# Optimization experiments

Hardware: AMD Instinct MI355X
Metric: run time of the kernel (lower is better)

## Reference

```python
import jax, jax.numpy as jnp
from jax import lax
import numpy as np

EPS_COS = 1e-8   # cosine-similarity eps (matches F.cosine_similarity default scale)
EPS_IN = 1e-5    # InstanceNorm2d default eps
NEG = -1e9


def _conv3(x, w, b):
    # x: [B,C,H,W], w: [O,I,3,3]
    y = lax.conv_general_dilated(x, w, (1, 1), 'SAME',
                                 dimension_numbers=('NCHW', 'OIHW', 'NCHW'))
    return y + b[None, :, None, None]


def _inorm(x):
    m = jnp.mean(x, axis=(2, 3), keepdims=True)
    v = jnp.var(x, axis=(2, 3), keepdims=True)
    return (x - m) * lax.rsqrt(v + EPS_IN)


def _shift(former, latter, mask):
    # former/latter: [B,C,H,W]; mask: [H,W] int (1 = hole).
    # For every masked pixel, find the most cosine-similar UNMASKED pixel in the
    # latter (known-region encoder) features and copy the former feature from it.
    B, C, H, W = former.shape
    L = H * W
    lat = lax.stop_gradient(latter).reshape(B, C, L)           # attention is non-differentiable
    latn = lat / (jnp.linalg.norm(lat, axis=1, keepdims=True) + EPS_COS)
    sim = jnp.einsum('bcm,bcn->bmn', latn, latn)               # [B,L,L] query m -> key n
    mflat = mask.reshape(L) > 0
    sim = jnp.where(mflat[None, None, :], NEG, sim)            # keys must be unmasked
    idx = jnp.argmax(sim, axis=-1)                             # [B,L]
    fflat = former.reshape(B, C, L)
    gathered = jnp.take_along_axis(fflat, jnp.broadcast_to(idx[:, None, :], (B, C, L)), axis=2)
    shift = jnp.where(mflat[None, None, :], gathered, 0.0)     # zeros outside the hole
    return shift.reshape(B, C, H, W)


def setup_inputs() -> dict:
    key = jax.random.key(0)
    ks = jax.random.split(key, 6)
    B, C, H, W = 8, 256, 64, 64
    inp = jax.random.normal(ks[0], (B, 2 * C, H, W), dtype=jnp.float32)
    mask = jax.random.randint(ks[1], (H, W), 0, 2, dtype=jnp.int32)
    s1 = 1.0 / float(np.sqrt(2 * C * 9))
    s2 = 1.0 / float(np.sqrt(C * 9))
    W1 = jax.random.uniform(ks[2], (C, 2 * C, 3, 3), jnp.float32, -s1, s1)
    b1 = jax.random.uniform(ks[3], (C,), jnp.float32, -s1, s1)
    W2 = jax.random.uniform(ks[4], (C, C, 3, 3), jnp.float32, -s2, s2)
    b2 = jax.random.uniform(ks[5], (C,), jnp.float32, -s2, s2)
    return {"input": inp, "mask": mask, "W1": W1, "b1": b1, "W2": W2, "b2": b2}


def reference(input, mask, W1, b1, W2, b2):
    C = input.shape[1] // 2
    F_c = input[:, :C]          # former (decoder) features
    F_s = input[:, C:]          # latter (encoder) features
    F_shift = _shift(F_c, F_s, mask)
    F_fuse = F_c * F_shift
    F_com = jnp.concatenate([F_c, F_fuse], axis=1)             # [B,2C,H,W]
    h = jax.nn.relu(_inorm(_conv3(F_com, W1, b1)))
    res = _inorm(_conv3(h, W2, b2))
    return jnp.concatenate([F_c + res, F_s], axis=1)
```

## Files before the change

### kernel.cpp

```cpp
#include <hip/hip_runtime.h>
#include <hip/hip_bf16.h>
#include <math.h>

#define L 4096
#define C 256
#define B 8

typedef __attribute__((ext_vector_type(8))) short bf16x8;
typedef __attribute__((ext_vector_type(8))) ushort u16x8;
typedef __attribute__((ext_vector_type(4))) float f32x4;

__device__ inline ushort f2bu(float f) { __hip_bfloat16 h = __float2bfloat16(f); return *(ushort*)&h; }
__device__ inline float bu2f(ushort u) { __hip_bfloat16 h; *(ushort*)&h = u; return __bfloat162float(h); }

#define SWZ(c) ((((c) >> 1) & 3) << 4)

__global__ __launch_bounds__(256) void compact_mask(
    const int* __restrict__ mask, int* __restrict__ counts,
    int* __restrict__ maskedOrig, int* __restrict__ unmaskOrig,
    int* __restrict__ posOf)
{
    __shared__ int smM[256], smU[256];
    int t = threadIdx.x;
    int flags[16];
    int cm = 0, cu = 0;
    for (int k = 0; k < 16; ++k) {
        int l = t * 16 + k;
        int f = mask[l] > 0;
        flags[k] = f;
        cm += f; cu += !f;
    }
    smM[t] = cm; smU[t] = cu;
    __syncthreads();
    for (int off = 1; off < 256; off <<= 1) {
        int vM = 0, vU = 0;
        if (t >= off) { vM = smM[t - off]; vU = smU[t - off]; }
        __syncthreads();
        smM[t] += vM; smU[t] += vU;
        __syncthreads();
    }
    if (t == 255) { counts[0] = smM[255]; counts[1] = smU[255]; }
    int pm = smM[t] - cm, pu = smU[t] - cu;
    for (int k = 0; k < 16; ++k) {
        int l = t * 16 + k;
        if (flags[k]) { maskedOrig[pm] = l; posOf[l] = pm; pm++; }
        else          { unmaskOrig[pu] = l; posOf[l] = pu; pu++; }
    }
}

__global__ __launch_bounds__(256) void norm_transpose(
    const float* __restrict__ input, const int* __restrict__ mask,
    const int* __restrict__ counts, const int* __restrict__ posOf,
    ushort* __restrict__ fsnh, ushort* __restrict__ fsnl)
{
    int bx = blockIdx.x;
    int b = bx >> 7;
    int l0 = (bx & 127) * 32;
    __shared__ float tile[256 * 33];
    __shared__ float part[8 * 33];
    __shared__ float denom[32];
    __shared__ int   rowdst[32];
    int t = threadIdx.x;
    int lsub = t & 31, cg = t >> 5;
    for (int cc = 0; cc < 256; cc += 8) {
        int c = cc + cg;
        tile[c * 33 + lsub] = input[((size_t)(b * 512 + 256 + c)) * L + l0 + lsub];
    }
    __syncthreads();
    float s = 0.f;
    for (int c = cg; c < 256; c += 8) { float v = tile[c * 33 + lsub]; s = fmaf(v, v, s); }
    part[cg * 33 + lsub] = s;
    __syncthreads();
    if (t < 32) {
        float s2 = 0.f;
        for (int g = 0; g < 8; ++g) s2 += part[g * 33 + t];
        denom[t] = sqrtf(s2) + 1e-8f;
        int l = l0 + t;
        int Nm = counts[0];
        rowdst[t] = (mask[l] > 0) ? posOf[l] : (Nm + posOf[l]);
    }
    __syncthreads();
    for (int ls = 0; ls < 32; ++ls) {
        int r = rowdst[ls];
        float d = denom[ls];
        float val = tile[t * 33 + ls] / d;
        ushort h = f2bu(val);
        float hf = bu2f(h);
        ushort lo = f2bu(val - hf);
        size_t o = ((size_t)b * L + r) * C + t;
        fsnh[o] = h;
        fsnl[o] = lo;
    }
}

__global__ __launch_bounds__(256, 2) void sim_argmax_v6(
    const ushort* __restrict__ hi, const ushort* __restrict__ lo,
    const int* __restrict__ counts,
    float* __restrict__ pval, int* __restrict__ pidx)
{
    __shared__ ushort ldsB[2 * 64 * 256];
    const int Nm = counts[0], Nu = counts[1];
    const int b = blockIdx.z;
    const int m0 = blockIdx.y * 64;
    const int half = blockIdx.x;
    const int t = threadIdx.x;
    const int w = t >> 6, l = t & 63;
    const int lm = l & 15, lk = l >> 4;
    const int key = lm << 4;

    const int nct = (Nu + 63) >> 6;
    const int hs = (nct + 1) >> 1;
    const int cA = half * hs, cB = half ? nct : hs;

    float bestv[4]; int bestn[4];
#pragma unroll
    for (int r = 0; r < 4; ++r) { bestv[r] = -3e38f; bestn[r] = 0; }

    if (m0 < Nm && cA < cB) {
        const char* bytesH = (const char*)hi;
        const char* bytesL = (const char*)lo;
        const size_t bL = (size_t)b * L;
        char* ldsc = (char*)ldsB;

#define STAGE(cc) do { \
    size_t gb = (bL + (size_t)Nm + (size_t)(cc) * 64) * 512; \
    _Pragma("unroll") \
    for (int i = 0; i < 8; ++i) { \
        int j = w * 8 + i; \
        int x = j * 1024 + l * 16; \
        int sx = x ^ (((x >> 9) & 15) << 4); \
        __builtin_amdgcn_global_load_lds((const __attribute__((address_space(1))) unsigned*)(bytesH + gb + sx), \
            (__attribute__((address_space(3))) unsigned*)(ldsc + j * 1024), 16, 0, 0); \
        __builtin_amdgcn_global_load_lds((const __attribute__((address_space(1))) unsigned*)(bytesL + gb + sx), \
            (__attribute__((address_space(3))) unsigned*)(ldsc + 32768 + j * 1024), 16, 0, 0); \
    } \
} while (0)

        STAGE(cA);

        const int rA = m0 + w * 16 + lm;
        bf16x8 ah[8], al[8];
        {
            const ushort* aH = hi + (bL + rA) * C + lk * 8;
            const ushort* aL = lo + (bL + rA) * C + lk * 8;
#pragma unroll
            for (int ks = 0; ks < 8; ++ks) {
                ah[ks] = *(const bf16x8*)(aH + ks * 32);
                al[ks] = *(const bf16x8*)(aL + ks * 32);
            }
        }

        for (int c = cA; c < cB; ++c) {
            asm volatile("s_waitcnt vmcnt(0)" ::: "memory");
            __syncthreads();
            f32x4 acc[4];
#pragma unroll
            for (int nf = 0; nf < 4; ++nf) acc[nf] = (f32x4){0.f, 0.f, 0.f, 0.f};
#pragma unroll
            for (int ks = 0; ks < 8; ++ks) {
                bf16x8 bh[4], bl[4];
#pragma unroll
                for (int nf = 0; nf < 4; ++nf) {
                    int row = nf * 16 + lm;
                    int addr = row * 512 + ((ks * 64 + lk * 16) ^ key);
                    bh[nf] = *(const bf16x8*)(ldsc + addr);
                    bl[nf] = *(const bf16x8*)(ldsc + 32768 + addr);
                }
#pragma unroll
                for (int nf = 0; nf < 4; ++nf)
                    acc[nf] = __builtin_amdgcn_mfma_f32_16x16x32_bf16(ah[ks], bh[nf], acc[nf], 0, 0, 0);
#pragma unroll
                for (int nf = 0; nf < 4; ++nf)
                    acc[nf] = __builtin_amdgcn_mfma_f32_16x16x32_bf16(ah[ks], bl[nf], acc[nf], 0, 0, 0);
#pragma unroll
                for (int nf = 0; nf < 4; ++nf)
                    acc[nf] = __builtin_amdgcn_mfma_f32_16x16x32_bf16(al[ks], bh[nf], acc[nf], 0, 0, 0);
            }
            __syncthreads();
            if (c + 1 < cB) STAGE(c + 1);
            int nbase = c * 64;
#pragma unroll
            for (int r = 0; r < 4; ++r) {
#pragma unroll
                for (int nf = 0; nf < 4; ++nf) {
                    int n = nbase + nf * 16 + lm;
                    float v = acc[nf][r];
                    if (n < Nu && v > bestv[r]) { bestv[r] = v; bestn[r] = n; }
                }
            }
        }
#undef STAGE
    }

    if (m0 >= Nm) return;
#pragma unroll
    for (int r = 0; r < 4; ++r) {
        float bv = bestv[r]; int bn = bestn[r];
#pragma unroll
        for (int mk = 1; mk < 16; mk <<= 1) {
            float ov = __shfl_xor(bv, mk, 64);
            int   on = __shfl_xor(bn, mk, 64);
            if (ov > bv || (ov == bv && on < bn)) { bv = ov; bn = on; }
        }
        if (lm == 0) {
            int m = m0 + w * 16 + lk * 4 + r;
            size_t o = ((size_t)(b * 4096 + m)) * 2 + half;
            pval[o] = bv; pidx[o] = bn;
        }
    }
}

__global__ __launch_bounds__(256) void wprep(
    const float* __restrict__ W1, const float* __restrict__ W2,
    ushort* __restrict__ W1bf, ushort* __restrict__ W2bf)
{
    int gid = blockIdx.x * 256 + threadIdx.x;
    const int N1 = 256 * 512 * 9;
    const int N2 = 256 * 256 * 9;
    if (gid < N1) {
        int ci = gid & 511; int rest = gid >> 9;
        int tau = rest % 9; int co = rest / 9;
        W1bf[gid] = f2bu(W1[((size_t)(co * 512 + ci)) * 9 + tau]);
    } else if (gid < N1 + N2) {
        int g = gid - N1;
        int ci = g & 255; int rest = g >> 8;
        int tau = rest % 9; int co = rest / 9;
        W2bf[g] = f2bu(W2[((size_t)(co * 256 + ci)) * 9 + tau]);
    }
}

__global__ __launch_bounds__(256) void in_prep1(
    const float* __restrict__ input, ushort* __restrict__ inT)
{
    int b = blockIdx.y;
    int p0 = blockIdx.x * 32;
    __shared__ float tile[256][33];
    int t = threadIdx.x;
    int pq = t & 7;
    for (int cc = 0; cc < 256; cc += 32) {
        int ci = cc + (t >> 3);
        float4 v = *(const float4*)(input + ((size_t)(b * 512 + ci)) * L + p0 + pq * 4);
        tile[ci][pq * 4 + 0] = v.x; tile[ci][pq * 4 + 1] = v.y;
        tile[ci][pq * 4 + 2] = v.z; tile[ci][pq * 4 + 3] = v.w;
    }
    __syncthreads();
    int c8 = t & 31;
    for (int pp = 0; pp < 32; pp += 8) {
        int pixloc = pp + (t >> 5);
        u16x8 u;
#pragma unroll
        for (int j = 0; j < 8; ++j) u[j] = f2bu(tile[c8 * 8 + j][pixloc]);
        *(u16x8*)(inT + ((size_t)(b * 4096 + p0 + pixloc)) * 512 + c8 * 8) = u;
    }
}

__global__ __launch_bounds__(256) void in_prep2(
    ushort* __restrict__ inT, const int* __restrict__ mask,
    const float* __restrict__ pval, const int* __restrict__ pidx,
    const int* __restrict__ posOf, const int* __restrict__ unmaskOrig)
{
    int gid = blockIdx.x * 256 + threadIdx.x;
    int c8 = gid & 31;
    int pix = (gid >> 5) & 4095;
    int b = gid >> 17;
    u16x8 out8;
    if (mask[pix] > 0) {
        int m = posOf[pix];
        size_t base = ((size_t)(b * 4096 + m)) * 2;
        float bv = pval[base]; int bn = pidx[base];
        float v1 = pval[base + 1]; int n1 = pidx[base + 1];
        if (v1 > bv || (v1 == bv && n1 < bn)) { bn = n1; }
        int n = unmaskOrig[bn];
        const ushort* rp = inT + ((size_t)(b * 4096 + pix)) * 512 + c8 * 8;
        const ushort* rn = inT + ((size_t)(b * 4096 + n)) * 512 + c8 * 8;
        u16x8 a = *(const u16x8*)rp;
        u16x8 bb = *(const u16x8*)rn;
#pragma unroll
        for (int j = 0; j < 8; ++j) out8[j] = f2bu(bu2f(a[j]) * bu2f(bb[j]));
    } else {
#pragma unroll
        for (int j = 0; j < 8; ++j) out8[j] = 0;
    }
    *(u16x8*)(inT + ((size_t)(b * 4096 + pix)) * 512 + 256 + c8 * 8) = out8;
}

template<int CKROW>
__global__ __launch_bounds__(256, 2) void conv_mfma(
    const ushort* __restrict__ Abf, const ushort* __restrict__ Wbf,
    float* __restrict__ outF, ushort* __restrict__ outH,
    float* __restrict__ psum, int store32)
{
    __shared__ float4 ldsv[62208 / 16];
    char* lds = (char*)ldsv;
    char* ldsB = lds + 25344;
    const int t = threadIdx.x;
    const int w = t >> 6;
    const int l = t & 63;
    const int lm = l & 15, lk = l >> 4;
    const int b = blockIdx.z;
    const int y0 = blockIdx.x * 4;
    const int c0 = blockIdx.y * 64;
    const int yw = y0 + w;
    const size_t abase = (size_t)b * 4096 * CKROW;

    f32x4 acc[4][4];
#pragma unroll
    for (int g = 0; g < 4; ++g)
#pragma unroll
        for (int nf = 0; nf < 4; ++nf) acc[g][nf] = (f32x4){0.f, 0.f, 0.f, 0.f};

    if (t < 48) {
        int r = t >> 3;
        int cX = ((t >> 2) & 1) ? 65 : 0;
        int k8 = t & 3;
        *(float4*)(lds + (r * 66 + cX) * 64 + ((k8 * 16) ^ SWZ(cX))) = (float4){0.f,0.f,0.f,0.f};
    }

    const int NKC = CKROW / 32;
    for (int kc = 0; kc < NKC; ++kc) {
        __syncthreads();
        {
            int x = t >> 2;
            int k8 = t & 3;
            int cX = x + 1;
            char* dbase = lds + cX * 64 + ((k8 * 16) ^ SWZ(cX));
#pragma unroll
            for (int r = 0; r < 6; ++r) {
                int yy = y0 - 1 + r;
                float4 v;
                if (yy >= 0 && yy < 64)
                    v = *(const float4*)(Abf + abase + (size_t)(yy * 64 + x) * CKROW + kc * 32 + k8 * 8);
                else
                    v = (float4){0.f, 0.f, 0.f, 0.f};
                *(float4*)(dbase + r * (66 * 64)) = v;
            }
        }
        {
            int cl = t >> 2;
            int k8 = t & 3;
            char* dbase = ldsB + cl * 64 + ((k8 * 16) ^ SWZ(cl));
            const ushort* sbase = Wbf + ((size_t)(c0 + cl) * 9) * CKROW + kc * 32 + k8 * 8;
#pragma unroll
            for (int tau = 0; tau < 9; ++tau) {
                *(float4*)(dbase + tau * (64 * 64)) = *(const float4*)(sbase + (size_t)tau * CKROW);
            }
        }
        __syncthreads();
#pragma unroll
        for (int ky = 0; ky < 3; ++ky) {
            int r = w + ky;
#pragma unroll
            for (int kx = 0; kx < 3; ++kx) {
                int tau = ky * 3 + kx;
                bf16x8 bfr[4];
#pragma unroll
                for (int nf = 0; nf < 4; ++nf) {
                    int cl = nf * 16 + lm;
                    bfr[nf] = *(bf16x8*)(ldsB + (tau * 64 + cl) * 64 + ((lk * 16) ^ SWZ(cl)));
                }
#pragma unroll
                for (int g = 0; g < 4; ++g) {
                    int cX = g * 16 + lm + kx;
                    bf16x8 afr = *(bf16x8*)(lds + (r * 66 + cX) * 64 + ((lk * 16) ^ SWZ(cX)));
#pragma unroll
                    for (int nf = 0; nf < 4; ++nf)
                        acc[g][nf] = __builtin_amdgcn_mfma_f32_16x16x32_bf16(afr, bfr[nf], acc[g][nf], 0, 0, 0);
                }
            }
        }
    }

    if (store32) {
#pragma unroll
        for (int g = 0; g < 4; ++g)
#pragma unroll
            for (int nf = 0; nf < 4; ++nf) {
                int cout = c0 + nf * 16 + lm;
#pragma unroll
                for (int r = 0; r < 4; ++r) {
                    int pix = yw * 64 + g * 16 + lk * 4 + r;
                    outF[((size_t)(b * 4096 + pix)) * 256 + cout] = acc[g][nf][r];
                }
            }
    } else {
#pragma unroll
        for (int g = 0; g < 4; ++g)
#pragma unroll
            for (int nf = 0; nf < 4; ++nf) {
                int cout = c0 + nf * 16 + lm;
#pragma unroll
                for (int r = 0; r < 4; ++r) {
                    int pix = yw * 64 + g * 16 + lk * 4 + r;
                    outH[((size_t)(b * 4096 + pix)) * 256 + cout] = f2bu(acc[g][nf][r]);
                }
            }
    }

    float s[4], q[4];
#pragma unroll
    for (int nf = 0; nf < 4; ++nf) {
        float ss = 0.f, qq = 0.f;
#pragma unroll
        for (int g = 0; g < 4; ++g)
#pragma unroll
            for (int r = 0; r < 4; ++r) { float v = acc[g][nf][r]; ss += v; qq = fmaf(v, v, qq); }
        ss += __shfl_xor(ss, 16, 64); ss += __shfl_xor(ss, 32, 64);
        qq += __shfl_xor(qq, 16, 64); qq += __shfl_xor(qq, 32, 64);
        s[nf] = ss; q[nf] = qq;
    }
    __syncthreads();
    float* S = (float*)lds;
    float* Q = (float*)(lds + 1024);
    if (l < 16) {
#pragma unroll
        for (int nf = 0; nf < 4; ++nf) {
            S[w * 64 + nf * 16 + l] = s[nf];
            Q[w * 64 + nf * 16 + l] = q[nf];
        }
    }
    __syncthreads();
    if (t < 64) {
        float ts = 0.f, tq = 0.f;
#pragma unroll
        for (int w2 = 0; w2 < 4; ++w2) { ts += S[w2 * 64 + t]; tq += Q[w2 * 64 + t]; }
        size_t o = (((size_t)(b * 256 + c0 + t)) * 16 + blockIdx.x) * 2;
        psum[o] = ts; psum[o + 1] = tq;
    }
}

__global__ __launch_bounds__(256) void stats_reduce(
    const float* __restrict__ psum, float* __restrict__ mrs)
{
    int b = blockIdx.x;
    int c = threadIdx.x;
    float s = 0.f, q = 0.f;
    size_t base = ((size_t)(b * 256 + c)) * 16;
    for (int k = 0; k < 16; ++k) { s += psum[(base + k) * 2]; q += psum[(base + k) * 2 + 1]; }
    float mean = s * (1.f / 4096.f);
    float var = q * (1.f / 4096.f) - mean * mean;
    float rs = rsqrtf(var + 1e-5f);
    mrs[(b * 256 + c) * 2] = mean;
    mrs[(b * 256 + c) * 2 + 1] = rs;
}

__global__ __launch_bounds__(256) void norm1_apply(
    const ushort* __restrict__ hraw, const float* __restrict__ mrs,
    ushort* __restrict__ hbf)
{
    int gid = blockIdx.x * 256 + threadIdx.x;
    int c8 = gid & 31;
    int pix = (gid >> 5) & 4095;
    int b = gid >> 17;
    size_t off = (((size_t)(b * 4096 + pix)) << 8) + c8 * 8;
    u16x8 v = *(const u16x8*)(hraw + off);
    const float* mb = mrs + (size_t)b * 512 + c8 * 16;
    u16x8 o;
#pragma unroll
    for (int j = 0; j < 8; ++j) {
        float z = (bu2f(v[j]) - mb[j * 2]) * mb[j * 2 + 1];
        o[j] = f2bu(z > 0.f ? z : 0.f);
    }
    *(u16x8*)(hbf + off) = o;
}

__global__ __launch_bounds__(256) void finalize_fs(
    const ushort* __restrict__ resbf, const float* __restrict__ mrs,
    const float* __restrict__ input, float* __restrict__ out)
{
    __shared__ float tileT[256][33];
    int bx = blockIdx.x;
    int t = threadIdx.x;
    if (bx < 8192) {
        size_t i = (size_t)bx * 256 + t;
        size_t b = i >> 18;
        size_t r = i & 262143;
        size_t o = ((size_t)(b * 512 + 256)) * 1024 + r;
        ((float4*)out)[o] = ((const float4*)input)[o];
        return;
    }
    int fb = bx - 8192;
    int b = fb >> 7;
    int p0 = (fb & 127) * 32;
    int c8 = t & 31;
    for (int pp = 0; pp < 32; pp += 8) {
        int pixloc = pp + (t >> 5);
        u16x8 u = *(const u16x8*)(resbf + (((size_t)(b * 4096 + p0 + pixloc)) << 8) + c8 * 8);
#pragma unroll
        for (int j = 0; j < 8; ++j) tileT[c8 * 8 + j][pixloc] = bu2f(u[j]);
    }
    __syncthreads();
    int pq = t & 7;
    for (int cc = 0; cc < 256; cc += 32) {
        int c = cc + (t >> 3);
        float m = mrs[(b * 256 + c) * 2];
        float rs = mrs[(b * 256 + c) * 2 + 1];
        size_t off = ((size_t)(b * 512 + c)) * L + p0 + pq * 4;
        float4 f = *(const float4*)(input + off);
        float4 o;
        o.x = f.x + (tileT[c][pq * 4 + 0] - m) * rs;
        o.y = f.y + (tileT[c][pq * 4 + 1] - m) * rs;
        o.z = f.z + (tileT[c][pq * 4 + 2] - m) * rs;
        o.w = f.w + (tileT[c][pq * 4 + 3] - m) * rs;
        *(float4*)(out + off) = o;
    }
}

extern "C" void kernel_launch(void* const* d_in, const int* in_sizes, int n_in,
                              void* d_out, int out_size, void* d_ws, size_t ws_size,
                              hipStream_t stream) {
    const float* input = (const float*)d_in[0];
    const int*   mask  = (const int*)d_in[1];
    const float* W1    = (const float*)d_in[2];
    const float* W2    = (const float*)d_in[4];
    float* out = (float*)d_out;
    (void)in_sizes; (void)n_in; (void)out_size; (void)ws_size;

    char* ob = (char*)d_out;
    char* wp = (char*)d_ws;

    ushort* fsnh = (ushort*)ob;
    ushort* fsnl = (ushort*)(ob + 16777216);
    float*  pval = (float*)(ob + 33554432);
    int*    pidx = (int*)(ob + 37748736);
    ushort* inT  = (ushort*)ob;
    ushort* hraw = (ushort*)(ob + 33554432);
    ushort* hbf  = (ushort*)ob;

    ushort* resbf  = (ushort*)wp;
    ushort* W1bf   = (ushort*)(wp + 16777216);
    ushort* W2bf   = (ushort*)(wp + 19136512);
    float*  psum1  = (float*)(wp + 20316160);
    float*  psum2  = (float*)(wp + 20578304);
    float*  mrs1   = (float*)(wp + 20840448);
    float*  mrs2   = (float*)(wp + 20856832);
    int* counts     = (int*)(wp + 20873216);
    int* maskedOrig = counts + 4;
    int* unmaskOrig = maskedOrig + L;
    int* posOf      = unmaskOrig + L;

    compact_mask<<<1, 256, 0, stream>>>(mask, counts, maskedOrig, unmaskOrig, posOf);
    norm_transpose<<<1024, 256, 0, stream>>>(input, mask, counts, posOf, fsnh, fsnl);
    sim_argmax_v6<<<dim3(2, 64, 8), 256, 0, stream>>>(fsnh, fsnl, counts, pval, pidx);
    wprep<<<6912, 256, 0, stream>>>(W1, W2, W1bf, W2bf);
    in_prep1<<<dim3(128, 8), 256, 0, stream>>>(input, inT);
    in_prep2<<<4096, 256, 0, stream>>>(inT, mask, pval, pidx, posOf, unmaskOrig);
    conv_mfma<512><<<dim3(16, 4, 8), 256, 0, stream>>>(inT, W1bf, (float*)nullptr, hraw, psum1, 0);
    stats_reduce<<<8, 256, 0, stream>>>(psum1, mrs1);
    norm1_apply<<<4096, 256, 0, stream>>>(hraw, mrs1, hbf);
    conv_mfma<256><<<dim3(16, 4, 8), 256, 0, stream>>>(hbf, W2bf, (float*)nullptr, resbf, psum2, 0);
    stats_reduce<<<8, 256, 0, stream>>>(psum2, mrs2);
    finalize_fs<<<9216, 256, 0, stream>>>(resbf, mrs2, input, out);
}
```

Measured before the change: 270.3 us.

## Register-prefetch next conv K-chunk and fuse instance-norm+ReLU into conv2 loads

Result: slower. 339.3 us (+25.5%).

```diff
diff --git a/kernel.cpp b/kernel.cpp
--- a/kernel.cpp
+++ b/kernel.cpp
@@ -284,11 +284,11 @@
     *(u16x8*)(inT + ((size_t)(b * 4096 + pix)) * 512 + 256 + c8 * 8) = out8;
 }
 
-template<int CKROW>
+template<int CKROW, int NORM_IN>
 __global__ __launch_bounds__(256, 2) void conv_mfma(
     const ushort* __restrict__ Abf, const ushort* __restrict__ Wbf,
-    float* __restrict__ outF, ushort* __restrict__ outH,
-    float* __restrict__ psum, int store32)
+    const float* __restrict__ mrsIn,
+    ushort* __restrict__ outH, float* __restrict__ psum)
 {
     __shared__ float4 ldsv[62208 / 16];
     char* lds = (char*)ldsv;
@@ -303,6 +303,10 @@
     const int yw = y0 + w;
     const size_t abase = (size_t)b * 4096 * CKROW;
 
+    const int x = t >> 2;
+    const int k8 = t & 3;
+    const int cX = x + 1;
+
     f32x4 acc[4][4];
 #pragma unroll
     for (int g = 0; g < 4; ++g)
@@ -311,41 +315,72 @@
 
     if (t < 48) {
         int r = t >> 3;
-        int cX = ((t >> 2) & 1) ? 65 : 0;
-        int k8 = t & 3;
-        *(float4*)(lds + (r * 66 + cX) * 64 + ((k8 * 16) ^ SWZ(cX))) = (float4){0.f,0.f,0.f,0.f};
-    }
+        int hX = ((t >> 2) & 1) ? 65 : 0;
+        int hk = t & 3;
+        *(float4*)(lds + (r * 66 + hX) * 64 + ((hk * 16) ^ SWZ(hX))) = (float4){0.f,0.f,0.f,0.f};
+    }
+
+    const ushort* wsrc = Wbf + ((size_t)(c0 + x) * 9) * CKROW + k8 * 8;
+    float4 Areg[6], Breg[9];
+#pragma unroll
+    for (int r = 0; r < 6; ++r) {
+        int yy = y0 - 1 + r;
+        Areg[r] = (yy >= 0 && yy < 64)
+            ? *(const float4*)(Abf + abase + (size_t)(yy * 64 + x) * CKROW + k8 * 8)
+            : (float4){0.f, 0.f, 0.f, 0.f};
+    }
+#pragma unroll
+    for (int tau = 0; tau < 9; ++tau)
+        Breg[tau] = *(const float4*)(wsrc + (size_t)tau * CKROW);
 
     const int NKC = CKROW / 32;
     for (int kc = 0; kc < NKC; ++kc) {
         __syncthreads();
         {
-            int x = t >> 2;
-            int k8 = t & 3;
-            int cX = x + 1;
             char* dbase = lds + cX * 64 + ((k8 * 16) ^ SWZ(cX));
+            if (NORM_IN) {
+                const float* mb = mrsIn + (size_t)b * 512 + (size_t)(kc * 32 + k8 * 8) * 2;
+                float mm[8], rr[8];
+#pragma unroll
+                for (int j = 0; j < 8; ++j) { mm[j] = mb[2 * j]; rr[j] = mb[2 * j + 1]; }
+#pragma unroll
+                for (int r = 0; r < 6; ++r) {
+                    int yy = y0 - 1 + r;
+                    float4 v = Areg[r];
+                    u16x8 u = *(u16x8*)&v;
+                    u16x8 o;
+#pragma unroll
+                    for (int j = 0; j < 8; ++j) {
+                        float z = (bu2f(u[j]) - mm[j]) * rr[j];
+                        o[j] = f2bu(z > 0.f ? z : 0.f);
+                    }
+                    float4 ov = *(float4*)&o;
+                    if (!(yy >= 0 && yy < 64)) ov = (float4){0.f, 0.f, 0.f, 0.f};
+                    *(float4*)(dbase + r * (66 * 64)) = ov;
+                }
+            } else {
+#pragma unroll
+                for (int r = 0; r < 6; ++r)
+                    *(float4*)(dbase + r * (66 * 64)) = Areg[r];
+            }
+            char* dbaseB = ldsB + x * 64 + ((k8 * 16) ^ SWZ(x));
+#pragma unroll
+            for (int tau = 0; tau < 9; ++tau)
+                *(float4*)(dbaseB + tau * (64 * 64)) = Breg[tau];
+        }
+        __syncthreads();
+        if (kc + 1 < NKC) {
 #pragma unroll
             for (int r = 0; r < 6; ++r) {
                 int yy = y0 - 1 + r;
-                float4 v;
-                if (yy >= 0 && yy < 64)
-                    v = *(const float4*)(Abf + abase + (size_t)(yy * 64 + x) * CKROW + kc * 32 + k8 * 8);
-                else
-                    v = (float4){0.f, 0.f, 0.f, 0.f};
-                *(float4*)(dbase + r * (66 * 64)) = v;
-            }
-        }
-        {
-            int cl = t >> 2;
-            int k8 = t & 3;
-            char* dbase = ldsB + cl * 64 + ((k8 * 16) ^ SWZ(cl));
-            const ushort* sbase = Wbf + ((size_t)(c0 + cl) * 9) * CKROW + kc * 32 + k8 * 8;
-#pragma unroll
-            for (int tau = 0; tau < 9; ++tau) {
-                *(float4*)(dbase + tau * (64 * 64)) = *(const float4*)(sbase + (size_t)tau * CKROW);
-            }
-        }
-        __syncthreads();
+                Areg[r] = (yy >= 0 && yy < 64)
+                    ? *(const float4*)(Abf + abase + (size_t)(yy * 64 + x) * CKROW + (kc + 1) * 32 + k8 * 8)
+                    : (float4){0.f, 0.f, 0.f, 0.f};
+            }
+#pragma unroll
+            for (int tau = 0; tau < 9; ++tau)
+                Breg[tau] = *(const float4*)(wsrc + (size_t)tau * CKROW + (kc + 1) * 32);
+        }
 #pragma unroll
         for (int ky = 0; ky < 3; ++ky) {
             int r = w + ky;
@@ -360,8 +395,8 @@
                 }
 #pragma unroll
                 for (int g = 0; g < 4; ++g) {
-                    int cX = g * 16 + lm + kx;
-                    bf16x8 afr = *(bf16x8*)(lds + (r * 66 + cX) * 64 + ((lk * 16) ^ SWZ(cX)));
+                    int aX = g * 16 + lm + kx;
+                    bf16x8 afr = *(bf16x8*)(lds + (r * 66 + aX) * 64 + ((lk * 16) ^ SWZ(aX)));
 #pragma unroll
                     for (int nf = 0; nf < 4; ++nf)
                         acc[g][nf] = __builtin_amdgcn_mfma_f32_16x16x32_bf16(afr, bfr[nf], acc[g][nf], 0, 0, 0);
@@ -370,31 +405,17 @@
         }
     }
 
-    if (store32) {
-#pragma unroll
-        for (int g = 0; g < 4; ++g)
-#pragma unroll
-            for (int nf = 0; nf < 4; ++nf) {
-                int cout = c0 + nf * 16 + lm;
-#pragma unroll
-                for (int r = 0; r < 4; ++r) {
-                    int pix = yw * 64 + g * 16 + lk * 4 + r;
-                    outF[((size_t)(b * 4096 + pix)) * 256 + cout] = acc[g][nf][r];
-                }
-            }
-    } else {
-#pragma unroll
-        for (int g = 0; g < 4; ++g)
-#pragma unroll
-            for (int nf = 0; nf < 4; ++nf) {
-                int cout = c0 + nf * 16 + lm;
-#pragma unroll
-                for (int r = 0; r < 4; ++r) {
-                    int pix = yw * 64 + g * 16 + lk * 4 + r;
-                    outH[((size_t)(b * 4096 + pix)) * 256 + cout] = f2bu(acc[g][nf][r]);
-                }
-            }
-    }
+#pragma unroll
+    for (int g = 0; g < 4; ++g)
+#pragma unroll
+        for (int nf = 0; nf < 4; ++nf) {
+            int cout = c0 + nf * 16 + lm;
+#pragma unroll
+            for (int r = 0; r < 4; ++r) {
+                int pix = yw * 64 + g * 16 + lk * 4 + r;
+                outH[((size_t)(b * 4096 + pix)) * 256 + cout] = f2bu(acc[g][nf][r]);
+            }
+        }
 
     float s[4], q[4];
 #pragma unroll
@@ -441,26 +462,6 @@
     float rs = rsqrtf(var + 1e-5f);
     mrs[(b * 256 + c) * 2] = mean;
     mrs[(b * 256 + c) * 2 + 1] = rs;
-}
-
-__global__ __launch_bounds__(256) void norm1_apply(
-    const ushort* __restrict__ hraw, const float* __restrict__ mrs,
-    ushort* __restrict__ hbf)
-{
-    int gid = blockIdx.x * 256 + threadIdx.x;
-    int c8 = gid & 31;
-    int pix = (gid >> 5) & 4095;
-    int b = gid >> 17;
-    size_t off = (((size_t)(b * 4096 + pix)) << 8) + c8 * 8;
-    u16x8 v = *(const u16x8*)(hraw + off);
-    const float* mb = mrs + (size_t)b * 512 + c8 * 16;
-    u16x8 o;
-#pragma unroll
-    for (int j = 0; j < 8; ++j) {
-        float z = (bu2f(v[j]) - mb[j * 2]) * mb[j * 2 + 1];
-        o[j] = f2bu(z > 0.f ? z : 0.f);
-    }
-    *(u16x8*)(hbf + off) = o;
 }
 
 __global__ __launch_bounds__(256) void finalize_fs(
@@ -524,7 +525,6 @@
     int*    pidx = (int*)(ob + 37748736);
     ushort* inT  = (ushort*)ob;
     ushort* hraw = (ushort*)(ob + 33554432);
-    ushort* hbf  = (ushort*)ob;
 
     ushort* resbf  = (ushort*)wp;
     ushort* W1bf   = (ushort*)(wp + 16777216);
@@ -544,10 +544,9 @@
     wprep<<<6912, 256, 0, stream>>>(W1, W2, W1bf, W2bf);
     in_prep1<<<dim3(128, 8), 256, 0, stream>>>(input, inT);
     in_prep2<<<4096, 256, 0, stream>>>(inT, mask, pval, pidx, posOf, unmaskOrig);
-    conv_mfma<512><<<dim3(16, 4, 8), 256, 0, stream>>>(inT, W1bf, (float*)nullptr, hraw, psum1, 0);
+    conv_mfma<512, 0><<<dim3(16, 4, 8), 256, 0, stream>>>(inT, W1bf, (const float*)nullptr, hraw, psum1);
     stats_reduce<<<8, 256, 0, stream>>>(psum1, mrs1);
-    norm1_apply<<<4096, 256, 0, stream>>>(hraw, mrs1, hbf);
-    conv_mfma<256><<<dim3(16, 4, 8), 256, 0, stream>>>(hbf, W2bf, (float*)nullptr, resbf, psum2, 0);
+    conv_mfma<256, 1><<<dim3(16, 4, 8), 256, 0, stream>>>(hraw, W2bf, mrs1, resbf, psum2);
     stats_reduce<<<8, 256, 0, stream>>>(psum2, mrs2);
     finalize_fs<<<9216, 256, 0, stream>>>(resbf, mrs2, input, out);
 }
```
